# Kernel tuning notes

Measured on AMD Instinct MI355X. Metric: run time of the kernel, lower is better.

Reference implementation:

```python
import jax, jax.numpy as jnp
import numpy as np

NM = 4096; NP = 4096; EM = 65536; EP = 65536; H = 256; HEADS = 4; G = 32


def _lin(k, din, dout):
    k1, k2 = jax.random.split(k)
    return (jax.random.normal(k1, (din, dout), jnp.float32) * (1.0 / np.sqrt(din)),
            jax.random.normal(k2, (dout,), jnp.float32) * 0.01)


def setup_inputs() -> dict:
    key = jax.random.key(0)
    ks = jax.random.split(key, 32)
    inp = {}
    inp['x_mol'] = jax.random.normal(ks[0], (NM, 8), jnp.float32)
    inp['x_prot'] = jax.random.normal(ks[1], (NP, 4), jnp.float32)
    inp['ea_mol'] = jax.random.normal(ks[2], (EM, 2), jnp.float32)
    inp['ea_prot'] = jax.random.normal(ks[3], (EP, 2), jnp.float32)
    inp['ei_mol'] = jax.random.randint(ks[4], (2, EM), 0, NM)
    inp['ei_prot'] = jax.random.randint(ks[5], (2, EP), 0, NP)
    inp['batch_mol'] = jnp.sort(jax.random.randint(ks[6], (NM,), 0, G))
    inp['batch_prot'] = jnp.sort(jax.random.randint(ks[7], (NP,), 0, G))
    inp['node_lin_mol_w'], inp['node_lin_mol_b'] = _lin(ks[8], 8, H)
    inp['node_lin_prot_w'], inp['node_lin_prot_b'] = _lin(ks[9], 4, H)
    inp['edge_lin_mol_w'], inp['edge_lin_mol_b'] = _lin(ks[10], 2, H)
    inp['edge_lin_prot_w'], inp['edge_lin_prot_b'] = _lin(ks[11], 2, H)
    # two GINE conv layers per graph, each with a 2-layer MLP; stack layer dim first
    for pref, base in (('mol', 12), ('prot', 16)):
        w1 = []; b1 = []; w2 = []; b2 = []
        for l in range(2):
            w, b = _lin(ks[base + 2 * l], H, H); w1.append(w); b1.append(b)
            w, b = _lin(ks[base + 2 * l + 1], H, H); w2.append(w); b2.append(b)
        inp[pref + '_w1'] = jnp.stack(w1); inp[pref + '_b1'] = jnp.stack(b1)
        inp[pref + '_w2'] = jnp.stack(w2); inp[pref + '_b2'] = jnp.stack(b2)
    for pref, base in (('mp', 20), ('pm', 23)):
        inp[pref + '_wq'], inp[pref + '_bq'] = _lin(ks[base], H, H)
        inp[pref + '_wk'], inp[pref + '_bk'] = _lin(ks[base + 1], H, H)
        inp[pref + '_wv'], inp[pref + '_bv'] = _lin(ks[base + 2], H, H)
    inp['fc1_w'], inp['fc1_b'] = _lin(ks[26], 2 * H, H)
    inp['fc2_w'], inp['fc2_b'] = _lin(ks[27], H, 1)
    return inp


def _gine_stack(x, ei, e, w1, b1, w2, b2):
    # GINEConv (eps=0): x_i' = relu(nn(x_i + sum_j relu(x_j + e_ji))), 2 layers, shared edge emb
    src, dst = ei[0], ei[1]
    n = x.shape[0]
    for l in range(w1.shape[0]):
        msg = jax.nn.relu(x[src] + e)                      # [E, H]
        agg = jax.ops.segment_sum(msg, dst, num_segments=n)  # [N, H]
        h = x + agg
        h = jax.nn.relu(h @ w1[l] + b1[l]) @ w2[l] + b2[l]
        x = jax.nn.relu(h)
    return x


def _cross_attn(qn, kn, wq, bq, wk, bk, wv, bv):
    nq, d = qn.shape
    nk = kn.shape[0]
    hd = d // HEADS
    Q = (qn @ wq + bq).reshape(nq, HEADS, hd)
    K = (kn @ wk + bk).reshape(nk, HEADS, hd)
    V = (kn @ wv + bv).reshape(nk, HEADS, hd)
    scores = jnp.einsum('qhd,khd->hqk', Q, K) / np.float32(hd ** 0.5)
    w = jax.nn.softmax(scores, axis=-1)
    return jnp.einsum('hqk,khd->qhd', w, V).reshape(nq, d)


def _seg_mean(h, seg, n):
    s = jax.ops.segment_sum(h, seg, num_segments=n)
    c = jax.ops.segment_sum(jnp.ones((h.shape[0], 1), h.dtype), seg, num_segments=n)
    return s / jnp.maximum(c, 1.0)


def reference(x_mol, x_prot, ea_mol, ea_prot, ei_mol, ei_prot, batch_mol, batch_prot,
              node_lin_mol_w, node_lin_mol_b, node_lin_prot_w, node_lin_prot_b,
              edge_lin_mol_w, edge_lin_mol_b, edge_lin_prot_w, edge_lin_prot_b,
              mol_w1, mol_b1, mol_w2, mol_b2, prot_w1, prot_b1, prot_w2, prot_b2,
              mp_wq, mp_bq, mp_wk, mp_bk, mp_wv, mp_bv,
              pm_wq, pm_bq, pm_wk, pm_bk, pm_wv, pm_bv,
              fc1_w, fc1_b, fc2_w, fc2_b):
    hm = x_mol @ node_lin_mol_w + node_lin_mol_b
    hp = x_prot @ node_lin_prot_w + node_lin_prot_b
    em = ea_mol @ edge_lin_mol_w + edge_lin_mol_b
    ep = ea_prot @ edge_lin_prot_w + edge_lin_prot_b
    H_mol = _gine_stack(hm, ei_mol, em, mol_w1, mol_b1, mol_w2, mol_b2)
    H_prot = _gine_stack(hp, ei_prot, ep, prot_w1, prot_b1, prot_w2, prot_b2)
    H_mol_c = H_mol + _cross_attn(H_mol, H_prot, mp_wq, mp_bq, mp_wk, mp_bk, mp_wv, mp_bv)
    H_prot_c = H_prot + _cross_attn(H_prot, H_mol, pm_wq, pm_bq, pm_wk, pm_bk, pm_wv, pm_bv)
    z_mol = _seg_mean(H_mol_c, batch_mol, G)
    z_prot = _seg_mean(H_prot_c, batch_prot, G)
    z = jnp.concatenate([z_mol, z_prot], axis=1)
    x = jax.nn.relu(z @ fc1_w + fc1_b)
    out = jax.nn.sigmoid(x @ fc2_w + fc2_b)
    return out.squeeze(-1)
```

## Files before the change

kernel.cpp:

```cpp
#include <hip/hip_runtime.h>
#include <math.h>

#define HDIM 256
#define NMOL 4096
#define NPROT 4096
#define NEDGE 65536
#define NG 32

typedef _Float16 f16x8 __attribute__((ext_vector_type(8)));
typedef _Float16 f16x4 __attribute__((ext_vector_type(4)));
typedef __attribute__((ext_vector_type(4))) float f32x4;

__device__ __forceinline__ void splitf(float x, _Float16& h, _Float16& l) {
  h = (_Float16)x;
  l = (_Float16)(x - (float)h);
}

struct PtrPack { const float* p[14]; };

__global__ __launch_bounds__(256) void k_prep_wt(PtrPack pk, _Float16* __restrict__ dh,
                                                 _Float16* __restrict__ dl) {
  __shared__ float Ts[64][68];
  const int m = blockIdx.z;
  const int n0 = blockIdx.y * 64, k0 = blockIdx.x * 64;
  const float* W = pk.p[m];
  const int t = threadIdx.x;
#pragma unroll
  for (int rep = 0; rep < 16; ++rep) {
    int k = rep * 4 + (t >> 6);
    int n = t & 63;
    Ts[n][k] = W[(size_t)(k0 + k) * 256 + n0 + n];
  }
  __syncthreads();
#pragma unroll
  for (int rep = 0; rep < 2; ++rep) {
    int idx = t + rep * 256;
    int nr = idx >> 3, koff = (idx & 7) * 8;
    f16x8 vh, vl;
#pragma unroll
    for (int i = 0; i < 8; ++i) {
      _Float16 h, l;
      splitf(Ts[nr][koff + i], h, l);
      vh[i] = h; vl[i] = l;
    }
    size_t off = (size_t)m * 65536 + (size_t)(n0 + nr) * 256 + k0 + koff;
    *(f16x8*)&dh[off] = vh;
    *(f16x8*)&dl[off] = vl;
  }
}

struct EmbJob {
  const float* x; const float* w; const float* b;
  _Float16* oh; _Float16* ol; int K;
};

__global__ __launch_bounds__(256) void k_node_embed2(EmbJob j0, EmbJob j1) {
  const EmbJob& j = blockIdx.y ? j1 : j0;
  const int i = blockIdx.x;
  const int c = threadIdx.x;
  float acc = j.b[c];
  for (int k = 0; k < j.K; ++k) acc += j.x[i * j.K + k] * j.w[k * HDIM + c];
  _Float16 h, l;
  splitf(acc, h, l);
  j.oh[(size_t)i * HDIM + c] = h;
  j.ol[(size_t)i * HDIM + c] = l;
}

__global__ __launch_bounds__(256) void k_csr_count2(const int* __restrict__ ei0,
                                                    const int* __restrict__ ei1,
                                                    int* __restrict__ cur0,
                                                    int* __restrict__ cur1, int E) {
  const int* ei = blockIdx.y ? ei1 : ei0;
  int* cur = blockIdx.y ? cur1 : cur0;
  const int e = blockIdx.x * 256 + threadIdx.x;
  if (e < E) atomicAdd(&cur[ei[E + e]], 1);
}

__global__ __launch_bounds__(256) void k_csr_scan2(int* __restrict__ c0, int* __restrict__ o0,
                                                   int* __restrict__ c1, int* __restrict__ o1,
                                                   int N) {
  int* cnt_cur = blockIdx.x ? c1 : c0;
  int* off = blockIdx.x ? o1 : o0;
  __shared__ int tsum[256], tpre[257];
  const int t = threadIdx.x;
  const int base = t * 16;
  int loc[16], s = 0;
#pragma unroll
  for (int i = 0; i < 16; ++i) { loc[i] = cnt_cur[base + i]; s += loc[i]; }
  tsum[t] = s;
  __syncthreads();
  if (t == 0) {
    int a = 0;
    for (int i = 0; i < 256; ++i) { tpre[i] = a; a += tsum[i]; }
    tpre[256] = a;
  }
  __syncthreads();
  int a = tpre[t];
#pragma unroll
  for (int i = 0; i < 16; ++i) {
    off[base + i] = a;
    cnt_cur[base + i] = a;
    a += loc[i];
  }
  if (t == 255) off[N] = tpre[256];
}

__global__ __launch_bounds__(256) void k_csr_scatter2(const int* __restrict__ ei0,
                                                      const int* __restrict__ ei1,
                                                      int* __restrict__ cur0,
                                                      int* __restrict__ cur1,
                                                      int* __restrict__ eid0,
                                                      int* __restrict__ eid1, int E) {
  const int* ei = blockIdx.y ? ei1 : ei0;
  int* cur = blockIdx.y ? cur1 : cur0;
  int* eid = blockIdx.y ? eid1 : eid0;
  const int e = blockIdx.x * 256 + threadIdx.x;
  if (e < E) {
    int pos = atomicAdd(&cur[ei[E + e]], 1);
    eid[pos] = e;
  }
}

struct AggJob {
  const _Float16* xh; const _Float16* xl; const float* ea;
  const int* eis; const int* off; const int* eid;
  const float* we; const float* be;
  _Float16* sh; _Float16* sl;
};

__global__ __launch_bounds__(256) void k_agg2(AggJob a0, AggJob a1) {
  const AggJob& a = blockIdx.y ? a1 : a0;
  const int n = blockIdx.x;
  const int c = threadIdx.x;
  const float w0 = a.we[c], w1 = a.we[HDIM + c], bb = a.be[c];
  const int j0 = a.off[n], j1 = a.off[n + 1];
  float sum = 0.f;
  for (int j = j0; j < j1; ++j) {
    int e = a.eid[j];
    int src = a.eis[e];
    float e0 = a.ea[2 * e], e1 = a.ea[2 * e + 1];
    float xv = (float)a.xh[(size_t)src * HDIM + c] + (float)a.xl[(size_t)src * HDIM + c];
    float m = xv + e0 * w0 + e1 * w1 + bb;
    sum += fmaxf(m, 0.f);
  }
  float self = (float)a.xh[(size_t)n * HDIM + c] + (float)a.xl[(size_t)n * HDIM + c];
  _Float16 h, l;
  splitf(self + sum, h, l);
  a.sh[(size_t)n * HDIM + c] = h;
  a.sl[(size_t)n * HDIM + c] = l;
}

struct GJob {
  const _Float16* Ah; const _Float16* Al;
  const _Float16* Bh; const _Float16* Bl;
  const float* bias;
  _Float16* Ch; _Float16* Cl; _Float16* Vt;
  float oscale; int flags;
};
struct GJobs { GJob j[6]; };

__global__ __launch_bounds__(256) void k_gemm(GJobs js) {
  const GJob J = js.j[blockIdx.z];
  const int relu = J.flags & 1;
  const int outmode = J.flags >> 4;
  __shared__ _Float16 Ah[64][72], Al[64][72], Bh[64][72], Bl[64][72];
  const int t = threadIdx.x;
  const int bm = blockIdx.x * 64, bn = blockIdx.y * 64;
  const int lane = t & 63, w = t >> 6;
  const int l15 = lane & 15, l4 = lane >> 4;
  const int wm = (w >> 1) * 32, wn = (w & 1) * 32;
  f32x4 acc[2][2] = {};
  for (int k0 = 0; k0 < 256; k0 += 64) {
    __syncthreads();
#pragma unroll
    for (int rep = 0; rep < 2; ++rep) {
      int idx = t + rep * 256;
      int r = idx >> 3, k8 = (idx & 7) * 8;
      size_t offa = (size_t)(bm + r) * 256 + k0 + k8;
      *(f16x8*)&Ah[r][k8] = *(const f16x8*)&J.Ah[offa];
      *(f16x8*)&Al[r][k8] = *(const f16x8*)&J.Al[offa];
      size_t offb = (size_t)(bn + r) * 256 + k0 + k8;
      *(f16x8*)&Bh[r][k8] = *(const f16x8*)&J.Bh[offb];
      *(f16x8*)&Bl[r][k8] = *(const f16x8*)&J.Bl[offb];
    }
    __syncthreads();
#pragma unroll
    for (int kh = 0; kh < 2; ++kh) {
      f16x8 a0h = *(f16x8*)&Ah[wm + l15][kh * 32 + l4 * 8];
      f16x8 a0l = *(f16x8*)&Al[wm + l15][kh * 32 + l4 * 8];
      f16x8 a1h = *(f16x8*)&Ah[wm + 16 + l15][kh * 32 + l4 * 8];
      f16x8 a1l = *(f16x8*)&Al[wm + 16 + l15][kh * 32 + l4 * 8];
      f16x8 b0h = *(f16x8*)&Bh[wn + l15][kh * 32 + l4 * 8];
      f16x8 b0l = *(f16x8*)&Bl[wn + l15][kh * 32 + l4 * 8];
      f16x8 b1h = *(f16x8*)&Bh[wn + 16 + l15][kh * 32 + l4 * 8];
      f16x8 b1l = *(f16x8*)&Bl[wn + 16 + l15][kh * 32 + l4 * 8];
      acc[0][0] = __builtin_amdgcn_mfma_f32_16x16x32_f16(a0h, b0h, acc[0][0], 0, 0, 0);
      acc[0][0] = __builtin_amdgcn_mfma_f32_16x16x32_f16(a0h, b0l, acc[0][0], 0, 0, 0);
      acc[0][0] = __builtin_amdgcn_mfma_f32_16x16x32_f16(a0l, b0h, acc[0][0], 0, 0, 0);
      acc[0][1] = __builtin_amdgcn_mfma_f32_16x16x32_f16(a0h, b1h, acc[0][1], 0, 0, 0);
      acc[0][1] = __builtin_amdgcn_mfma_f32_16x16x32_f16(a0h, b1l, acc[0][1], 0, 0, 0);
      acc[0][1] = __builtin_amdgcn_mfma_f32_16x16x32_f16(a0l, b1h, acc[0][1], 0, 0, 0);
      acc[1][0] = __builtin_amdgcn_mfma_f32_16x16x32_f16(a1h, b0h, acc[1][0], 0, 0, 0);
      acc[1][0] = __builtin_amdgcn_mfma_f32_16x16x32_f16(a1h, b0l, acc[1][0], 0, 0, 0);
      acc[1][0] = __builtin_amdgcn_mfma_f32_16x16x32_f16(a1l, b0h, acc[1][0], 0, 0, 0);
      acc[1][1] = __builtin_amdgcn_mfma_f32_16x16x32_f16(a1h, b1h, acc[1][1], 0, 0, 0);
      acc[1][1] = __builtin_amdgcn_mfma_f32_16x16x32_f16(a1h, b1l, acc[1][1], 0, 0, 0);
      acc[1][1] = __builtin_amdgcn_mfma_f32_16x16x32_f16(a1l, b1h, acc[1][1], 0, 0, 0);
    }
  }
  if (outmode == 3) __syncthreads();
#pragma unroll
  for (int mi = 0; mi < 2; ++mi)
#pragma unroll
    for (int ni = 0; ni < 2; ++ni) {
      int col = bn + wn + ni * 16 + l15;
      float bv = J.bias[col];
#pragma unroll
      for (int r = 0; r < 4; ++r) {
        int row = bm + wm + mi * 16 + l4 * 4 + r;
        float v = acc[mi][ni][r] + bv;
        if (relu) v = fmaxf(v, 0.f);
        if (outmode == 1) {
          float vs = v * J.oscale;
          _Float16 hh, ll;
          splitf(vs, hh, ll);
          J.Ch[(size_t)row * 256 + col] = hh;
          J.Cl[(size_t)row * 256 + col] = ll;
        } else {
          Ah[wn + ni * 16 + l15][wm + mi * 16 + l4 * 4 + r] = (_Float16)v;
        }
      }
    }
  if (outmode == 3) {
    __syncthreads();
#pragma unroll
    for (int rep = 0; rep < 2; ++rep) {
      int idx = t + rep * 256;
      int d = idx >> 3, n8 = (idx & 7) * 8;
      *(f16x8*)&J.Vt[(size_t)(bn + d) * 4096 + bm + n8] = *(f16x8*)&Ah[d][n8];
    }
  }
}

struct AttnArgs {
  const _Float16* Qh[2]; const _Float16* Ql[2];
  const _Float16* Kh[2]; const _Float16* Kl[2];
  const _Float16* Vth[2];
  float* Opart; float* mpart; float* lpart;
};

__global__ __launch_bounds__(256) void k_attn4(AttnArgs A, int nk_half) {
  __shared__ _Float16 Ksh[64][72], Ksl[64][72];
  __shared__ _Float16 Vsh[64][72];
  __shared__ _Float16 Psh[4][16][72];
  const int t = threadIdx.x;
  const int dir = blockIdx.y >> 2, h = blockIdx.y & 3;
  const int q0 = blockIdx.x * 64;
  const int half = blockIdx.z;
  const int kbase = half * nk_half;
  const int lane = t & 63, w = t >> 6;
  const int l15 = lane & 15, l4 = lane >> 4;

  const _Float16* Qh_g = A.Qh[dir];
  const _Float16* Ql_g = A.Ql[dir];
  const _Float16* Kh_g = A.Kh[dir];
  const _Float16* Kl_g = A.Kl[dir];
  const _Float16* Vth_g = A.Vth[dir];

  f16x8 qh[2], ql[2];
  {
    size_t qoff = (size_t)(q0 + w * 16 + l15) * 256 + h * 64;
#pragma unroll
    for (int kh = 0; kh < 2; ++kh) {
      qh[kh] = *(const f16x8*)&Qh_g[qoff + kh * 32 + l4 * 8];
      ql[kh] = *(const f16x8*)&Ql_g[qoff + kh * 32 + l4 * 8];
    }
  }
  f32x4 o[4] = {};
  float mrun = -1e30f;
  float lrun = 0.f;

  for (int kt = 0; kt < nk_half; kt += 64) {
    const int k0 = kbase + kt;
    __syncthreads();
#pragma unroll
    for (int rep = 0; rep < 2; ++rep) {
      int idx = t + rep * 256;
      int r = idx >> 3, c8 = idx & 7;
      size_t koff = (size_t)(k0 + r) * 256 + h * 64 + c8 * 8;
      *(f16x8*)&Ksh[r][c8 * 8] = *(const f16x8*)&Kh_g[koff];
      *(f16x8*)&Ksl[r][c8 * 8] = *(const f16x8*)&Kl_g[koff];
      int sc = c8 ^ ((r >> 3) & 7);
      size_t voff = (size_t)(h * 64 + r) * 4096 + k0 + c8 * 8;
      *(f16x8*)&Vsh[r][sc * 8] = *(const f16x8*)&Vth_g[voff];
    }
    __syncthreads();

    f32x4 sf[4] = {};
#pragma unroll
    for (int kc = 0; kc < 4; ++kc) {
      f16x8 kf0h = *(f16x8*)&Ksh[kc * 16 + l15][l4 * 8];
      f16x8 kf0l = *(f16x8*)&Ksl[kc * 16 + l15][l4 * 8];
      f16x8 kf1h = *(f16x8*)&Ksh[kc * 16 + l15][32 + l4 * 8];
      f16x8 kf1l = *(f16x8*)&Ksl[kc * 16 + l15][32 + l4 * 8];
      sf[kc] = __builtin_amdgcn_mfma_f32_16x16x32_f16(kf0h, qh[0], sf[kc], 0, 0, 0);
      sf[kc] = __builtin_amdgcn_mfma_f32_16x16x32_f16(kf0h, ql[0], sf[kc], 0, 0, 0);
      sf[kc] = __builtin_amdgcn_mfma_f32_16x16x32_f16(kf0l, qh[0], sf[kc], 0, 0, 0);
      sf[kc] = __builtin_amdgcn_mfma_f32_16x16x32_f16(kf1h, qh[1], sf[kc], 0, 0, 0);
      sf[kc] = __builtin_amdgcn_mfma_f32_16x16x32_f16(kf1h, ql[1], sf[kc], 0, 0, 0);
      sf[kc] = __builtin_amdgcn_mfma_f32_16x16x32_f16(kf1l, qh[1], sf[kc], 0, 0, 0);
    }

    float mt = -1e30f;
#pragma unroll
    for (int kc = 0; kc < 4; ++kc) {
      float a = fmaxf(fmaxf(sf[kc][0], sf[kc][1]), fmaxf(sf[kc][2], sf[kc][3]));
      mt = fmaxf(mt, a);
    }
    mt = fmaxf(mt, __shfl_xor(mt, 16, 64));
    mt = fmaxf(mt, __shfl_xor(mt, 32, 64));
    float mn = fmaxf(mrun, mt);
    float alpha = __expf(mrun - mn);
    mrun = mn;
    float rs = 0.f;
    _Float16 pf[4][4];
#pragma unroll
    for (int kc = 0; kc < 4; ++kc)
#pragma unroll
      for (int r = 0; r < 4; ++r) {
        float pv = __expf(sf[kc][r] - mn);
        rs += pv;
        pf[kc][r] = (_Float16)pv;
      }
    rs += __shfl_xor(rs, 16, 64);
    rs += __shfl_xor(rs, 32, 64);
    lrun = lrun * alpha + rs;

#pragma unroll
    for (int r = 0; r < 4; ++r) {
      float ar = __shfl(alpha, 4 * l4 + r, 64);
      o[0][r] *= ar; o[1][r] *= ar; o[2][r] *= ar; o[3][r] *= ar;
    }

#pragma unroll
    for (int kc = 0; kc < 4; ++kc) {
      f16x4 pv = {pf[kc][0], pf[kc][1], pf[kc][2], pf[kc][3]};
      *(f16x4*)&Psh[w][l15][kc * 16 + 4 * l4] = pv;
    }

#pragma unroll
    for (int kh = 0; kh < 2; ++kh) {
      f16x8 pa = *(f16x8*)&Psh[w][l15][kh * 32 + l4 * 8];
#pragma unroll
      for (int oc = 0; oc < 4; ++oc) {
        int d = oc * 16 + l15;
        int chunk = (kh * 4 + l4) ^ ((d >> 3) & 7);
        f16x8 vb = *(f16x8*)&Vsh[d][chunk * 8];
        o[oc] = __builtin_amdgcn_mfma_f32_16x16x32_f16(pa, vb, o[oc], 0, 0, 0);
      }
    }
  }

  const int slot = dir * 2 + half;
#pragma unroll
  for (int oc = 0; oc < 4; ++oc) {
    int col = h * 64 + oc * 16 + l15;
#pragma unroll
    for (int r = 0; r < 4; ++r) {
      int row = q0 + w * 16 + 4 * l4 + r;
      A.Opart[((size_t)slot * 4096 + row) * 256 + col] = o[oc][r];
    }
  }
  if (lane < 16) {
    int row = q0 + w * 16 + l15;
    A.mpart[(size_t)(slot * 4 + h) * 4096 + row] = mrun;
    A.lpart[(size_t)(slot * 4 + h) * 4096 + row] = lrun;
  }
}

__global__ __launch_bounds__(256) void k_combine_pool(
    const float* __restrict__ Opart, const float* __restrict__ mpart,
    const float* __restrict__ lpart,
    const _Float16* __restrict__ hmh, const _Float16* __restrict__ hml,
    const _Float16* __restrict__ hph, const _Float16* __restrict__ hpl,
    const int* __restrict__ b_mol, const int* __restrict__ b_prot,
    float* __restrict__ z, float* __restrict__ cnt) {
  const int row = blockIdx.x;
  const int dir = blockIdx.y;
  const int c = threadIdx.x;
  const int h = c >> 6;
  const _Float16* Hh = dir ? hph : hmh;
  const _Float16* Hl = dir ? hpl : hml;
  const int g = (dir ? b_prot : b_mol)[row];
  size_t mi0 = (size_t)((dir * 2 + 0) * 4 + h) * 4096 + row;
  size_t mi1 = (size_t)((dir * 2 + 1) * 4 + h) * 4096 + row;
  float m1 = mpart[mi0], m2 = mpart[mi1];
  float l1 = lpart[mi0], l2 = lpart[mi1];
  float M = fmaxf(m1, m2);
  float e1 = __expf(m1 - M), e2 = __expf(m2 - M);
  float L = l1 * e1 + l2 * e2;
  float O1 = Opart[((size_t)(dir * 2 + 0) * 4096 + row) * 256 + c];
  float O2 = Opart[((size_t)(dir * 2 + 1) * 4096 + row) * 256 + c];
  float hin = (float)Hh[(size_t)row * 256 + c] + (float)Hl[(size_t)row * 256 + c];
  float v = (O1 * e1 + O2 * e2) / L + hin;
  atomicAdd(&z[(size_t)g * 512 + dir * 256 + c], v);
  if (c == 0) atomicAdd(&cnt[dir * 32 + g], 1.0f);
}

__global__ __launch_bounds__(256) void k_segdiv(float* __restrict__ z,
                                                const float* __restrict__ cnt) {
  const int idx = blockIdx.x * 256 + threadIdx.x;
  const int g = idx >> 9, c = idx & 511;
  const float cc = cnt[(c < 256) ? g : (32 + g)];
  z[idx] /= fmaxf(cc, 1.0f);
}

__global__ __launch_bounds__(256) void k_fc1(
    const float* __restrict__ z, const float* __restrict__ w,
    const float* __restrict__ b, float* __restrict__ out) {
  const int idx = blockIdx.x * 256 + threadIdx.x;
  const int r = idx >> 8, c = idx & 255;
  float acc = b[c];
  for (int k = 0; k < 512; ++k) acc += z[r * 512 + k] * w[k * HDIM + c];
  out[idx] = fmaxf(acc, 0.f);
}

__global__ __launch_bounds__(64) void k_fc2(
    const float* __restrict__ xin, const float* __restrict__ w,
    const float* __restrict__ b, float* __restrict__ out) {
  const int r = threadIdx.x;
  if (r < NG) {
    float acc = b[0];
    for (int k = 0; k < HDIM; ++k) acc += xin[r * HDIM + k] * w[k];
    out[r] = 1.0f / (1.0f + __expf(-acc));
  }
}

extern "C" void kernel_launch(void* const* d_in, const int* in_sizes, int n_in,
                              void* d_out, int out_size, void* d_ws, size_t ws_size,
                              hipStream_t stream) {
  const float* x_mol   = (const float*)d_in[0];
  const float* x_prot  = (const float*)d_in[1];
  const float* ea_mol  = (const float*)d_in[2];
  const float* ea_prot = (const float*)d_in[3];
  const int*   ei_mol  = (const int*)d_in[4];
  const int*   ei_prot = (const int*)d_in[5];
  const int*   b_mol   = (const int*)d_in[6];
  const int*   b_prot  = (const int*)d_in[7];
  const float* nlm_w = (const float*)d_in[8];
  const float* nlm_b = (const float*)d_in[9];
  const float* nlp_w = (const float*)d_in[10];
  const float* nlp_b = (const float*)d_in[11];
  const float* elm_w = (const float*)d_in[12];
  const float* elm_b = (const float*)d_in[13];
  const float* elp_w = (const float*)d_in[14];
  const float* elp_b = (const float*)d_in[15];
  const float* mol_w1 = (const float*)d_in[16];
  const float* mol_b1 = (const float*)d_in[17];
  const float* mol_w2 = (const float*)d_in[18];
  const float* mol_b2 = (const float*)d_in[19];
  const float* prot_w1 = (const float*)d_in[20];
  const float* prot_b1 = (const float*)d_in[21];
  const float* prot_w2 = (const float*)d_in[22];
  const float* prot_b2 = (const float*)d_in[23];
  const float* mp_wq = (const float*)d_in[24];
  const float* mp_bq = (const float*)d_in[25];
  const float* mp_wk = (const float*)d_in[26];
  const float* mp_bk = (const float*)d_in[27];
  const float* mp_wv = (const float*)d_in[28];
  const float* mp_bv = (const float*)d_in[29];
  const float* pm_wq = (const float*)d_in[30];
  const float* pm_bq = (const float*)d_in[31];
  const float* pm_wk = (const float*)d_in[32];
  const float* pm_bk = (const float*)d_in[33];
  const float* pm_wv = (const float*)d_in[34];
  const float* pm_bv = (const float*)d_in[35];
  const float* fc1_w = (const float*)d_in[36];
  const float* fc1_b = (const float*)d_in[37];
  const float* fc2_w = (const float*)d_in[38];
  const float* fc2_b = (const float*)d_in[39];
  float* out = (float*)d_out;

  char* W8 = (char*)d_ws;
  const size_t MB = 1u << 20;
  _Float16* wtH  = (_Float16*)(W8 + 0 * MB);
  _Float16* wtL  = (_Float16*)(W8 + 2 * MB);
  _Float16* hmh  = (_Float16*)(W8 + 4 * MB);
  _Float16* hml  = (_Float16*)(W8 + 6 * MB);
  _Float16* hph  = (_Float16*)(W8 + 8 * MB);
  _Float16* hpl  = (_Float16*)(W8 + 10 * MB);
  _Float16* amh  = (_Float16*)(W8 + 12 * MB);
  _Float16* aml  = (_Float16*)(W8 + 14 * MB);
  _Float16* aph  = (_Float16*)(W8 + 16 * MB);
  _Float16* apl  = (_Float16*)(W8 + 18 * MB);
  _Float16* t1mh = (_Float16*)(W8 + 20 * MB);
  _Float16* t1ml = (_Float16*)(W8 + 22 * MB);
  _Float16* t1ph = (_Float16*)(W8 + 24 * MB);
  _Float16* t1pl = (_Float16*)(W8 + 26 * MB);
  _Float16* Qh0  = (_Float16*)(W8 + 28 * MB);
  _Float16* Ql0  = (_Float16*)(W8 + 30 * MB);
  _Float16* Kh0  = (_Float16*)(W8 + 32 * MB);
  _Float16* Kl0  = (_Float16*)(W8 + 34 * MB);
  _Float16* Qh1  = (_Float16*)(W8 + 36 * MB);
  _Float16* Ql1  = (_Float16*)(W8 + 38 * MB);
  _Float16* Kh1  = (_Float16*)(W8 + 40 * MB);
  _Float16* Kl1  = (_Float16*)(W8 + 42 * MB);
  _Float16* Vth0 = (_Float16*)(W8 + 44 * MB);
  _Float16* Vth1 = (_Float16*)(W8 + 46 * MB);
  float* Opart = (float*)(W8 + 48 * MB);
  float* mpart = (float*)(W8 + 64 * MB);
  float* lpart = mpart + 65536;
  float* zb    = lpart + 65536;
  float* cnt   = zb + 32 * 512;
  float* fch   = cnt + 64;
  int* off_m = (int*)(W8 + 65 * MB);
  int* cur_m = off_m + 4224;
  int* eid_m = cur_m + 4224;
  int* off_p = (int*)(W8 + 66 * MB);
  int* cur_p = off_p + 4224;
  int* eid_p = cur_p + 4224;

  PtrPack pk;
  pk.p[0] = mol_w1;           pk.p[1] = mol_w1 + 65536;
  pk.p[2] = mol_w2;           pk.p[3] = mol_w2 + 65536;
  pk.p[4] = prot_w1;          pk.p[5] = prot_w1 + 65536;
  pk.p[6] = prot_w2;          pk.p[7] = prot_w2 + 65536;
  pk.p[8] = mp_wq;  pk.p[9] = mp_wk;  pk.p[10] = mp_wv;
  pk.p[11] = pm_wq; pk.p[12] = pm_wk; pk.p[13] = pm_wv;
  k_prep_wt<<<dim3(4, 4, 14), 256, 0, stream>>>(pk, wtH, wtL);

  hipMemsetAsync(cur_m, 0, 4096 * 4, stream);
  hipMemsetAsync(cur_p, 0, 4096 * 4, stream);
  k_csr_count2<<<dim3(NEDGE / 256, 2), 256, 0, stream>>>(ei_mol, ei_prot, cur_m, cur_p, NEDGE);
  k_csr_scan2<<<2, 256, 0, stream>>>(cur_m, off_m, cur_p, off_p, NMOL);
  k_csr_scatter2<<<dim3(NEDGE / 256, 2), 256, 0, stream>>>(ei_mol, ei_prot, cur_m, cur_p,
                                                           eid_m, eid_p, NEDGE);

  EmbJob em = {x_mol, nlm_w, nlm_b, hmh, hml, 8};
  EmbJob ep = {x_prot, nlp_w, nlp_b, hph, hpl, 4};
  k_node_embed2<<<dim3(NMOL, 2), 256, 0, stream>>>(em, ep);

#define WTH(i) (wtH + (size_t)(i) * 65536)
#define WTL(i) (wtL + (size_t)(i) * 65536)

  AggJob am = {hmh, hml, ea_mol, ei_mol, off_m, eid_m, elm_w, elm_b, amh, aml};
  AggJob ap = {hph, hpl, ea_prot, ei_prot, off_p, eid_p, elp_w, elp_b, aph, apl};

  for (int l = 0; l < 2; ++l) {
    k_agg2<<<dim3(NMOL, 2), 256, 0, stream>>>(am, ap);
    GJobs g1 = {};
    g1.j[0] = {amh, aml, WTH(l), WTL(l), mol_b1 + l * 256,
               t1mh, t1ml, nullptr, 1.0f, 1 | (1 << 4)};
    g1.j[1] = {aph, apl, WTH(4 + l), WTL(4 + l), prot_b1 + l * 256,
               t1ph, t1pl, nullptr, 1.0f, 1 | (1 << 4)};
    k_gemm<<<dim3(64, 4, 2), 256, 0, stream>>>(g1);
    GJobs g2 = {};
    g2.j[0] = {t1mh, t1ml, WTH(2 + l), WTL(2 + l), mol_b2 + l * 256,
               hmh, hml, nullptr, 1.0f, 1 | (1 << 4)};
    g2.j[1] = {t1ph, t1pl, WTH(6 + l), WTL(6 + l), prot_b2 + l * 256,
               hph, hpl, nullptr, 1.0f, 1 | (1 << 4)};
    k_gemm<<<dim3(64, 4, 2), 256, 0, stream>>>(g2);
  }

  {
    GJobs q = {};
    q.j[0] = {hmh, hml, WTH(8), WTL(8), mp_bq, Qh0, Ql0, nullptr, 0.125f, 1 << 4};
    q.j[1] = {hph, hpl, WTH(9), WTL(9), mp_bk, Kh0, Kl0, nullptr, 1.0f, 1 << 4};
    q.j[2] = {hph, hpl, WTH(10), WTL(10), mp_bv, nullptr, nullptr, Vth0, 1.0f, 3 << 4};
    q.j[3] = {hph, hpl, WTH(11), WTL(11), pm_bq, Qh1, Ql1, nullptr, 0.125f, 1 << 4};
    q.j[4] = {hmh, hml, WTH(12), WTL(12), pm_bk, Kh1, Kl1, nullptr, 1.0f, 1 << 4};
    q.j[5] = {hmh, hml, WTH(13), WTL(13), pm_bv, nullptr, nullptr, Vth1, 1.0f, 3 << 4};
    k_gemm<<<dim3(64, 4, 6), 256, 0, stream>>>(q);
  }

  AttnArgs aa;
  aa.Qh[0] = Qh0; aa.Ql[0] = Ql0; aa.Kh[0] = Kh0; aa.Kl[0] = Kl0; aa.Vth[0] = Vth0;
  aa.Qh[1] = Qh1; aa.Ql[1] = Ql1; aa.Kh[1] = Kh1; aa.Kl[1] = Kl1; aa.Vth[1] = Vth1;
  aa.Opart = Opart; aa.mpart = mpart; aa.lpart = lpart;
  k_attn4<<<dim3(64, 8, 2), 256, 0, stream>>>(aa, 2048);

  hipMemsetAsync(zb, 0, (32 * 512 + 64) * 4, stream);
  k_combine_pool<<<dim3(4096, 2), 256, 0, stream>>>(Opart, mpart, lpart,
                                                    hmh, hml, hph, hpl,
                                                    b_mol, b_prot, zb, cnt);
  k_segdiv<<<64, 256, 0, stream>>>(zb, cnt);
  k_fc1<<<32, 256, 0, stream>>>(zb, fc1_w, fc1_b, fch);
  k_fc2<<<1, 64, 0, stream>>>(fch, fc2_w, fc2_b, out);
#undef WTH
#undef WTL
}
```

Before: 535.2 us.

## Double attention query tile, pack edge records for aggregation, fuse MLP head

The attention kernel now handles 32 query rows per wave (128 per block). Each K/V tile loaded into shared memory is therefore reused for twice as many queries, while the grid shrinks by half. The CSR build writes packed 16-byte edge records (source, two attributes), removing the eid-based indirection in aggregation, and the aggregation loop is unrolled by two. The segment division, fc1 and fc2 kernels are fused into one head kernel to cut launches. The larger attention tile raises register pressure and lowers block count, which may reduce occupancy.

```diff
diff --git a/kernel.cpp b/kernel.cpp
--- a/kernel.cpp
+++ b/kernel.cpp
@@ -15,6 +15,8 @@
   h = (_Float16)x;
   l = (_Float16)(x - (float)h);
 }
+
+struct __align__(16) EdgeRec { int src; float a0; float a1; int pad; };
 
 struct PtrPack { const float* p[14]; };
 
@@ -105,26 +107,30 @@
   if (t == 255) off[N] = tpre[256];
 }
 
-__global__ __launch_bounds__(256) void k_csr_scatter2(const int* __restrict__ ei0,
-                                                      const int* __restrict__ ei1,
-                                                      int* __restrict__ cur0,
-                                                      int* __restrict__ cur1,
-                                                      int* __restrict__ eid0,
-                                                      int* __restrict__ eid1, int E) {
+__global__ __launch_bounds__(256) void k_csr_scatter2(
+    const int* __restrict__ ei0, const int* __restrict__ ei1,
+    const float* __restrict__ ea0, const float* __restrict__ ea1,
+    int* __restrict__ cur0, int* __restrict__ cur1,
+    EdgeRec* __restrict__ er0, EdgeRec* __restrict__ er1, int E) {
   const int* ei = blockIdx.y ? ei1 : ei0;
+  const float* ea = blockIdx.y ? ea1 : ea0;
   int* cur = blockIdx.y ? cur1 : cur0;
-  int* eid = blockIdx.y ? eid1 : eid0;
+  EdgeRec* er = blockIdx.y ? er1 : er0;
   const int e = blockIdx.x * 256 + threadIdx.x;
   if (e < E) {
     int pos = atomicAdd(&cur[ei[E + e]], 1);
-    eid[pos] = e;
+    EdgeRec r;
+    r.src = ei[e];
+    r.a0 = ea[2 * e];
+    r.a1 = ea[2 * e + 1];
+    r.pad = 0;
+    er[pos] = r;
   }
 }
 
 struct AggJob {
-  const _Float16* xh; const _Float16* xl; const float* ea;
-  const int* eis; const int* off; const int* eid;
-  const float* we; const float* be;
+  const _Float16* xh; const _Float16* xl; const EdgeRec* er;
+  const int* off; const float* we; const float* be;
   _Float16* sh; _Float16* sl;
 };
 
@@ -135,13 +141,19 @@
   const float w0 = a.we[c], w1 = a.we[HDIM + c], bb = a.be[c];
   const int j0 = a.off[n], j1 = a.off[n + 1];
   float sum = 0.f;
-  for (int j = j0; j < j1; ++j) {
-    int e = a.eid[j];
-    int src = a.eis[e];
-    float e0 = a.ea[2 * e], e1 = a.ea[2 * e + 1];
-    float xv = (float)a.xh[(size_t)src * HDIM + c] + (float)a.xl[(size_t)src * HDIM + c];
-    float m = xv + e0 * w0 + e1 * w1 + bb;
-    sum += fmaxf(m, 0.f);
+  int j = j0;
+  for (; j + 1 < j1; j += 2) {
+    EdgeRec ra = a.er[j];
+    EdgeRec rb = a.er[j + 1];
+    float xa = (float)a.xh[(size_t)ra.src * HDIM + c] + (float)a.xl[(size_t)ra.src * HDIM + c];
+    float xb = (float)a.xh[(size_t)rb.src * HDIM + c] + (float)a.xl[(size_t)rb.src * HDIM + c];
+    sum += fmaxf(xa + ra.a0 * w0 + ra.a1 * w1 + bb, 0.f);
+    sum += fmaxf(xb + rb.a0 * w0 + rb.a1 * w1 + bb, 0.f);
+  }
+  if (j < j1) {
+    EdgeRec ra = a.er[j];
+    float xa = (float)a.xh[(size_t)ra.src * HDIM + c] + (float)a.xl[(size_t)ra.src * HDIM + c];
+    sum += fmaxf(xa + ra.a0 * w0 + ra.a1 * w1 + bb, 0.f);
   }
   float self = (float)a.xh[(size_t)n * HDIM + c] + (float)a.xl[(size_t)n * HDIM + c];
   _Float16 h, l;
@@ -249,17 +261,18 @@
   float* Opart; float* mpart; float* lpart;
 };
 
-__global__ __launch_bounds__(256) void k_attn4(AttnArgs A, int nk_half) {
+__global__ __launch_bounds__(256) void k_attn5(AttnArgs A, int nk_half) {
   __shared__ _Float16 Ksh[64][72], Ksl[64][72];
   __shared__ _Float16 Vsh[64][72];
-  __shared__ _Float16 Psh[4][16][72];
+  __shared__ _Float16 Psh[4][32][72];
   const int t = threadIdx.x;
   const int dir = blockIdx.y >> 2, h = blockIdx.y & 3;
-  const int q0 = blockIdx.x * 64;
+  const int q0 = blockIdx.x * 128;
   const int half = blockIdx.z;
   const int kbase = half * nk_half;
   const int lane = t & 63, w = t >> 6;
   const int l15 = lane & 15, l4 = lane >> 4;
+  const int qw = q0 + w * 32;
 
   const _Float16* Qh_g = A.Qh[dir];
   const _Float16* Ql_g = A.Ql[dir];
@@ -267,18 +280,19 @@
   const _Float16* Kl_g = A.Kl[dir];
   const _Float16* Vth_g = A.Vth[dir];
 
-  f16x8 qh[2], ql[2];
-  {
-    size_t qoff = (size_t)(q0 + w * 16 + l15) * 256 + h * 64;
+  f16x8 qh[2][2], ql[2][2];
+#pragma unroll
+  for (int qf = 0; qf < 2; ++qf) {
+    size_t qoff = (size_t)(qw + qf * 16 + l15) * 256 + h * 64;
 #pragma unroll
     for (int kh = 0; kh < 2; ++kh) {
-      qh[kh] = *(const f16x8*)&Qh_g[qoff + kh * 32 + l4 * 8];
-      ql[kh] = *(const f16x8*)&Ql_g[qoff + kh * 32 + l4 * 8];
-    }
-  }
-  f32x4 o[4] = {};
-  float mrun = -1e30f;
-  float lrun = 0.f;
+      qh[qf][kh] = *(const f16x8*)&Qh_g[qoff + kh * 32 + l4 * 8];
+      ql[qf][kh] = *(const f16x8*)&Ql_g[qoff + kh * 32 + l4 * 8];
+    }
+  }
+  f32x4 o[2][4] = {};
+  float mrun[2] = {-1e30f, -1e30f};
+  float lrun[2] = {0.f, 0.f};
 
   for (int kt = 0; kt < nk_half; kt += 64) {
     const int k0 = kbase + kt;
@@ -296,85 +310,94 @@
     }
     __syncthreads();
 
-    f32x4 sf[4] = {};
+    f32x4 sf[2][4] = {};
 #pragma unroll
     for (int kc = 0; kc < 4; ++kc) {
       f16x8 kf0h = *(f16x8*)&Ksh[kc * 16 + l15][l4 * 8];
       f16x8 kf0l = *(f16x8*)&Ksl[kc * 16 + l15][l4 * 8];
       f16x8 kf1h = *(f16x8*)&Ksh[kc * 16 + l15][32 + l4 * 8];
       f16x8 kf1l = *(f16x8*)&Ksl[kc * 16 + l15][32 + l4 * 8];
-      sf[kc] = __builtin_amdgcn_mfma_f32_16x16x32_f16(kf0h, qh[0], sf[kc], 0, 0, 0);
-      sf[kc] = __builtin_amdgcn_mfma_f32_16x16x32_f16(kf0h, ql[0], sf[kc], 0, 0, 0);
-      sf[kc] = __builtin_amdgcn_mfma_f32_16x16x32_f16(kf0l, qh[0], sf[kc], 0, 0, 0);
-      sf[kc] = __builtin_amdgcn_mfma_f32_16x16x32_f16(kf1h, qh[1], sf[kc], 0, 0, 0);
-      sf[kc] = __builtin_amdgcn_mfma_f32_16x16x32_f16(kf1h, ql[1], sf[kc], 0, 0, 0);
-      sf[kc] = __builtin_amdgcn_mfma_f32_16x16x32_f16(kf1l, qh[1], sf[kc], 0, 0, 0);
-    }
-
-    float mt = -1e30f;
-#pragma unroll
-    for (int kc = 0; kc < 4; ++kc) {
-      float a = fmaxf(fmaxf(sf[kc][0], sf[kc][1]), fmaxf(sf[kc][2], sf[kc][3]));
-      mt = fmaxf(mt, a);
-    }
-    mt = fmaxf(mt, __shfl_xor(mt, 16, 64));
-    mt = fmaxf(mt, __shfl_xor(mt, 32, 64));
-    float mn = fmaxf(mrun, mt);
-    float alpha = __expf(mrun - mn);
-    mrun = mn;
-    float rs = 0.f;
-    _Float16 pf[4][4];
-#pragma unroll
-    for (int kc = 0; kc < 4; ++kc)
+#pragma unroll
+      for (int qf = 0; qf < 2; ++qf) {
+        sf[qf][kc] = __builtin_amdgcn_mfma_f32_16x16x32_f16(kf0h, qh[qf][0], sf[qf][kc], 0, 0, 0);
+        sf[qf][kc] = __builtin_amdgcn_mfma_f32_16x16x32_f16(kf0h, ql[qf][0], sf[qf][kc], 0, 0, 0);
+        sf[qf][kc] = __builtin_amdgcn_mfma_f32_16x16x32_f16(kf0l, qh[qf][0], sf[qf][kc], 0, 0, 0);
+        sf[qf][kc] = __builtin_amdgcn_mfma_f32_16x16x32_f16(kf1h, qh[qf][1], sf[qf][kc], 0, 0, 0);
+        sf[qf][kc] = __builtin_amdgcn_mfma_f32_16x16x32_f16(kf1h, ql[qf][1], sf[qf][kc], 0, 0, 0);
+        sf[qf][kc] = __builtin_amdgcn_mfma_f32_16x16x32_f16(kf1l, qh[qf][1], sf[qf][kc], 0, 0, 0);
+      }
+    }
+
+#pragma unroll
+    for (int qf = 0; qf < 2; ++qf) {
+      float mt = -1e30f;
+#pragma unroll
+      for (int kc = 0; kc < 4; ++kc) {
+        float a = fmaxf(fmaxf(sf[qf][kc][0], sf[qf][kc][1]),
+                        fmaxf(sf[qf][kc][2], sf[qf][kc][3]));
+        mt = fmaxf(mt, a);
+      }
+      mt = fmaxf(mt, __shfl_xor(mt, 16, 64));
+      mt = fmaxf(mt, __shfl_xor(mt, 32, 64));
+      float mn = fmaxf(mrun[qf], mt);
+      float alpha = __expf(mrun[qf] - mn);
+      mrun[qf] = mn;
+      float rs = 0.f;
+#pragma unroll
+      for (int kc = 0; kc < 4; ++kc) {
+        float p0 = __expf(sf[qf][kc][0] - mn);
+        float p1 = __expf(sf[qf][kc][1] - mn);
+        float p2 = __expf(sf[qf][kc][2] - mn);
+        float p3 = __expf(sf[qf][kc][3] - mn);
+        rs += (p0 + p1) + (p2 + p3);
+        f16x4 pv = {(_Float16)p0, (_Float16)p1, (_Float16)p2, (_Float16)p3};
+        *(f16x4*)&Psh[w][qf * 16 + l15][kc * 16 + 4 * l4] = pv;
+      }
+      rs += __shfl_xor(rs, 16, 64);
+      rs += __shfl_xor(rs, 32, 64);
+      lrun[qf] = lrun[qf] * alpha + rs;
 #pragma unroll
       for (int r = 0; r < 4; ++r) {
-        float pv = __expf(sf[kc][r] - mn);
-        rs += pv;
-        pf[kc][r] = (_Float16)pv;
+        float ar = __shfl(alpha, 4 * l4 + r, 64);
+        o[qf][0][r] *= ar; o[qf][1][r] *= ar;
+        o[qf][2][r] *= ar; o[qf][3][r] *= ar;
       }
-    rs += __shfl_xor(rs, 16, 64);
-    rs += __shfl_xor(rs, 32, 64);
-    lrun = lrun * alpha + rs;
-
-#pragma unroll
-    for (int r = 0; r < 4; ++r) {
-      float ar = __shfl(alpha, 4 * l4 + r, 64);
-      o[0][r] *= ar; o[1][r] *= ar; o[2][r] *= ar; o[3][r] *= ar;
-    }
-
-#pragma unroll
-    for (int kc = 0; kc < 4; ++kc) {
-      f16x4 pv = {pf[kc][0], pf[kc][1], pf[kc][2], pf[kc][3]};
-      *(f16x4*)&Psh[w][l15][kc * 16 + 4 * l4] = pv;
     }
 
 #pragma unroll
     for (int kh = 0; kh < 2; ++kh) {
-      f16x8 pa = *(f16x8*)&Psh[w][l15][kh * 32 + l4 * 8];
+      f16x8 pa0 = *(f16x8*)&Psh[w][l15][kh * 32 + l4 * 8];
+      f16x8 pa1 = *(f16x8*)&Psh[w][16 + l15][kh * 32 + l4 * 8];
 #pragma unroll
       for (int oc = 0; oc < 4; ++oc) {
         int d = oc * 16 + l15;
         int chunk = (kh * 4 + l4) ^ ((d >> 3) & 7);
         f16x8 vb = *(f16x8*)&Vsh[d][chunk * 8];
-        o[oc] = __builtin_amdgcn_mfma_f32_16x16x32_f16(pa, vb, o[oc], 0, 0, 0);
+        o[0][oc] = __builtin_amdgcn_mfma_f32_16x16x32_f16(pa0, vb, o[0][oc], 0, 0, 0);
+        o[1][oc] = __builtin_amdgcn_mfma_f32_16x16x32_f16(pa1, vb, o[1][oc], 0, 0, 0);
       }
     }
   }
 
   const int slot = dir * 2 + half;
 #pragma unroll
-  for (int oc = 0; oc < 4; ++oc) {
-    int col = h * 64 + oc * 16 + l15;
-#pragma unroll
-    for (int r = 0; r < 4; ++r) {
-      int row = q0 + w * 16 + 4 * l4 + r;
-      A.Opart[((size_t)slot * 4096 + row) * 256 + col] = o[oc][r];
-    }
-  }
+  for (int qf = 0; qf < 2; ++qf)
+#pragma unroll
+    for (int oc = 0; oc < 4; ++oc) {
+      int col = h * 64 + oc * 16 + l15;
+#pragma unroll
+      for (int r = 0; r < 4; ++r) {
+        int row = qw + qf * 16 + 4 * l4 + r;
+        A.Opart[((size_t)slot * 4096 + row) * 256 + col] = o[qf][oc][r];
+      }
+    }
   if (lane < 16) {
-    int row = q0 + w * 16 + l15;
-    A.mpart[(size_t)(slot * 4 + h) * 4096 + row] = mrun;
-    A.lpart[(size_t)(slot * 4 + h) * 4096 + row] = lrun;
+#pragma unroll
+    for (int qf = 0; qf < 2; ++qf) {
+      int row = qw + qf * 16 + l15;
+      A.mpart[(size_t)(slot * 4 + h) * 4096 + row] = mrun[qf];
+      A.lpart[(size_t)(slot * 4 + h) * 4096 + row] = lrun[qf];
+    }
   }
 }
 
@@ -407,32 +430,28 @@
   if (c == 0) atomicAdd(&cnt[dir * 32 + g], 1.0f);
 }
 
-__global__ __launch_bounds__(256) void k_segdiv(float* __restrict__ z,
-                                                const float* __restrict__ cnt) {
-  const int idx = blockIdx.x * 256 + threadIdx.x;
-  const int g = idx >> 9, c = idx & 511;
-  const float cc = cnt[(c < 256) ? g : (32 + g)];
-  z[idx] /= fmaxf(cc, 1.0f);
-}
-
-__global__ __launch_bounds__(256) void k_fc1(
-    const float* __restrict__ z, const float* __restrict__ w,
-    const float* __restrict__ b, float* __restrict__ out) {
-  const int idx = blockIdx.x * 256 + threadIdx.x;
-  const int r = idx >> 8, c = idx & 255;
-  float acc = b[c];
-  for (int k = 0; k < 512; ++k) acc += z[r * 512 + k] * w[k * HDIM + c];
-  out[idx] = fmaxf(acc, 0.f);
-}
-
-__global__ __launch_bounds__(64) void k_fc2(
-    const float* __restrict__ xin, const float* __restrict__ w,
-    const float* __restrict__ b, float* __restrict__ out) {
-  const int r = threadIdx.x;
-  if (r < NG) {
-    float acc = b[0];
-    for (int k = 0; k < HDIM; ++k) acc += xin[r * HDIM + k] * w[k];
-    out[r] = 1.0f / (1.0f + __expf(-acc));
+__global__ __launch_bounds__(256) void k_head(
+    const float* __restrict__ z, const float* __restrict__ cnt,
+    const float* __restrict__ w1, const float* __restrict__ b1,
+    const float* __restrict__ w2, const float* __restrict__ b2,
+    float* __restrict__ out) {
+  __shared__ float wsum[4];
+  const int r = blockIdx.x;
+  const int c = threadIdx.x;
+  const float im = 1.0f / fmaxf(cnt[r], 1.0f);
+  const float ip = 1.0f / fmaxf(cnt[32 + r], 1.0f);
+  float acc = b1[c];
+  for (int k = 0; k < 256; ++k) acc += (z[r * 512 + k] * im) * w1[k * HDIM + c];
+  for (int k = 256; k < 512; ++k) acc += (z[r * 512 + k] * ip) * w1[k * HDIM + c];
+  acc = fmaxf(acc, 0.f);
+  float p = acc * w2[c];
+#pragma unroll
+  for (int off = 1; off < 64; off <<= 1) p += __shfl_xor(p, off, 64);
+  if ((c & 63) == 0) wsum[c >> 6] = p;
+  __syncthreads();
+  if (c == 0) {
+    float s = (wsum[0] + wsum[1]) + (wsum[2] + wsum[3]) + b2[0];
+    out[r] = 1.0f / (1.0f + __expf(-s));
   }
 }
 
@@ -512,13 +531,12 @@
   float* lpart = mpart + 65536;
   float* zb    = lpart + 65536;
   float* cnt   = zb + 32 * 512;
-  float* fch   = cnt + 64;
   int* off_m = (int*)(W8 + 65 * MB);
   int* cur_m = off_m + 4224;
-  int* eid_m = cur_m + 4224;
   int* off_p = (int*)(W8 + 66 * MB);
   int* cur_p = off_p + 4224;
-  int* eid_p = cur_p + 4224;
+  EdgeRec* er_m = (EdgeRec*)(W8 + 67 * MB);
+  EdgeRec* er_p = (EdgeRec*)(W8 + 68 * MB);
 
   PtrPack pk;
   pk.p[0] = mol_w1;           pk.p[1] = mol_w1 + 65536;
@@ -533,8 +551,8 @@
   hipMemsetAsync(cur_p, 0, 4096 * 4, stream);
   k_csr_count2<<<dim3(NEDGE / 256, 2), 256, 0, stream>>>(ei_mol, ei_prot, cur_m, cur_p, NEDGE);
   k_csr_scan2<<<2, 256, 0, stream>>>(cur_m, off_m, cur_p, off_p, NMOL);
-  k_csr_scatter2<<<dim3(NEDGE / 256, 2), 256, 0, stream>>>(ei_mol, ei_prot, cur_m, cur_p,
-                                                           eid_m, eid_p, NEDGE);
+  k_csr_scatter2<<<dim3(NEDGE / 256, 2), 256, 0, stream>>>(ei_mol, ei_prot, ea_mol, ea_prot,
+                                                           cur_m, cur_p, er_m, er_p, NEDGE);
 
   EmbJob em = {x_mol, nlm_w, nlm_b, hmh, hml, 8};
   EmbJob ep = {x_prot, nlp_w, nlp_b, hph, hpl, 4};
@@ -543,8 +561,8 @@
 #define WTH(i) (wtH + (size_t)(i) * 65536)
 #define WTL(i) (wtL + (size_t)(i) * 65536)
 
-  AggJob am = {hmh, hml, ea_mol, ei_mol, off_m, eid_m, elm_w, elm_b, amh, aml};
-  AggJob ap = {hph, hpl, ea_prot, ei_prot, off_p, eid_p, elp_w, elp_b, aph, apl};
+  AggJob am = {hmh, hml, er_m, off_m, elm_w, elm_b, amh, aml};
+  AggJob ap = {hph, hpl, er_p, off_p, elp_w, elp_b, aph, apl};
 
   for (int l = 0; l < 2; ++l) {
     k_agg2<<<dim3(NMOL, 2), 256, 0, stream>>>(am, ap);
@@ -577,15 +595,13 @@
   aa.Qh[0] = Qh0; aa.Ql[0] = Ql0; aa.Kh[0] = Kh0; aa.Kl[0] = Kl0; aa.Vth[0] = Vth0;
   aa.Qh[1] = Qh1; aa.Ql[1] = Ql1; aa.Kh[1] = Kh1; aa.Kl[1] = Kl1; aa.Vth[1] = Vth1;
   aa.Opart = Opart; aa.mpart = mpart; aa.lpart = lpart;
-  k_attn4<<<dim3(64, 8, 2), 256, 0, stream>>>(aa, 2048);
+  k_attn5<<<dim3(32, 8, 2), 256, 0, stream>>>(aa, 2048);
 
   hipMemsetAsync(zb, 0, (32 * 512 + 64) * 4, stream);
   k_combine_pool<<<dim3(4096, 2), 256, 0, stream>>>(Opart, mpart, lpart,
                                                     hmh, hml, hph, hpl,
                                                     b_mol, b_prot, zb, cnt);
-  k_segdiv<<<64, 256, 0, stream>>>(zb, cnt);
-  k_fc1<<<32, 256, 0, stream>>>(zb, fc1_w, fc1_b, fch);
-  k_fc2<<<1, 64, 0, stream>>>(fch, fc2_w, fc2_b, out);
+  k_head<<<NG, 256, 0, stream>>>(zb, cnt, fc1_w, fc1_b, fc2_w, fc2_b, out);
 #undef WTH
 #undef WTL
 }
```

Result: faster. 501.7 us (-6.2%).
